# Performance work log

Measured on AMD Instinct MI355X. Metric: run time of the kernel, lower is better.

Reference implementation:

```python
import jax, jax.numpy as jnp
import numpy as np

NUM_TASKS = 5
POOL = 5
R = 8
TOPK = 3
SCALE = 1.0  # module self.scale and forward scale arg, both 1
B, S, DIN, DOUT = 4, 4096, 1024, 1024


def setup_inputs() -> dict:
    key = jax.random.key(0)
    ks = jax.random.split(key, 5)
    inp = {
        "input": jax.random.normal(ks[0], (B, S, DIN), dtype=jnp.float32),
        "W": jax.random.normal(ks[1], (DOUT, DIN), dtype=jnp.float32) / np.sqrt(DIN),
        "lora_down": jax.random.normal(ks[2], (POOL, DIN, R), dtype=jnp.float32) / np.sqrt(DIN),
        "lora_up": jax.random.normal(ks[3], (POOL, R, DOUT), dtype=jnp.float32) / np.sqrt(R),
        "lora_route": jax.random.normal(ks[4], (NUM_TASKS, DIN, POOL), dtype=jnp.float32) * 0.02,
        "task_id": 4,
    }
    return inp


def reference(input, W, lora_down, lora_up, lora_route, task_id):
    # Eval branch (self.training == False), 1 <= task_id <= num_tasks.
    task_id = min(task_id, NUM_TASKS)
    k = min(task_id, TOPK)
    route = lora_route[1]                          # [DIN, POOL] (detach split is a no-op for fwd)
    input_mean = jnp.mean(input, axis=1)           # [B, DIN]
    lora_omegas = jnp.mean(input_mean @ route, axis=0)  # [POOL]
    sliced = lora_omegas[1:task_id + 1]            # source slices from 1
    G, I = jax.lax.top_k(sliced, k)                # indices used DIRECTLY (as in source)
    gate = jax.nn.softmax(G)                       # [k]
    # detached expert products (eval path detaches lora_down @ lora_up)
    dw = jax.lax.stop_gradient(
        jnp.einsum('kdr,kro->kdo', lora_down[I], lora_up[I]))  # [k, DIN, DOUT]
    # delta = sum_i gate[i] * SCALE * (input @ dw[i]); forward scale arg = 1
    delta = SCALE * jnp.einsum('k,bsd,kdo->bso', gate, input, dw)
    # delta_w_all[:B//2] = 0
    bmask = (jnp.arange(input.shape[0]) >= input.shape[0] // 2).astype(delta.dtype)
    delta = delta * bmask[:, None, None]
    return input @ W.T + delta
```

## Files before the change

### kernel.cpp

```cpp
#include <hip/hip_runtime.h>
#include <hip/hip_bf16.h>

typedef __attribute__((ext_vector_type(8))) __bf16 bf16x8;
typedef __attribute__((ext_vector_type(4))) __bf16 bf16x4;
typedef __attribute__((ext_vector_type(4))) float f32x4;

#define DIN 1024
#define DOUT 1024
#define BB 4
#define SS 4096
#define MROWS (BB*SS)
#define POOLN 5
#define RR 8
#define NTASKS 5
#define TOPKK 3

__global__ __launch_bounds__(256) void kA_colsum(const float* __restrict__ in,
                                                 float* __restrict__ partial) {
    const int t = threadIdx.x;
    const int b = blockIdx.x;
    const int idx0 = b * 256 + t;
    const f32x4* __restrict__ inv = (const f32x4*)in;

    float s0 = 0.f, s1 = 0.f, s2 = 0.f, s3 = 0.f;
    size_t idx = idx0;
    f32x4 cur = inv[idx];
#pragma unroll
    for (int i = 0; i < 8; ++i) {
        f32x4 nxt = cur;
        if (i < 7) nxt = inv[idx + 524288];
        s0 += cur[0]; s1 += cur[1]; s2 += cur[2]; s3 += cur[3];
        cur = nxt;
        idx += 524288;
    }
    const int c0 = (t * 4) & (DIN - 1);
    f32x4 p = { s0, s1, s2, s3 };
    *(f32x4*)&partial[(size_t)b * DIN + c0] = p;
}

__global__ __launch_bounds__(256) void k1b_reduce(const float* __restrict__ partial,
                                                  float* __restrict__ partial2) {
    const int tid = blockIdx.x * 256 + threadIdx.x;
    const int c = tid & (DIN - 1);
    const int g = tid >> 10;
    float s = 0.f;
    const int r0 = g * 256;
#pragma unroll 8
    for (int r = r0; r < r0 + 256; ++r)
        s += partial[(size_t)r * DIN + c];
    partial2[(size_t)g * DIN + c] = s;
}

__global__ void k2_gate(const float* __restrict__ partial2,
                        const float* __restrict__ lroute,
                        const int* __restrict__ task_id_p,
                        float* __restrict__ gate, int* __restrict__ gidx) {
    __shared__ float red[4][POOLN];
    const int tix = threadIdx.x;
    const int w = tix >> 6, l = tix & 63;
    float part[POOLN] = {0.f, 0.f, 0.f, 0.f, 0.f};
    for (int d = w * 256 + l; d < w * 256 + 256; d += 64) {
        float cs = 0.f;
#pragma unroll
        for (int g = 0; g < 8; ++g) cs += partial2[g * DIN + d];
        cs *= (1.0f / (float)MROWS);
        const float* rp = &lroute[(size_t)1 * DIN * POOLN + (size_t)d * POOLN];
#pragma unroll
        for (int p = 0; p < POOLN; ++p) part[p] += cs * rp[p];
    }
#pragma unroll
    for (int p = 0; p < POOLN; ++p) {
        float v = part[p];
        for (int off = 32; off; off >>= 1) v += __shfl_down(v, off);
        if (l == 0) red[w][p] = v;
    }
    __syncthreads();
    if (tix == 0) {
#pragma unroll
        for (int p = 0; p < POOLN; ++p)
            part[p] = red[0][p] + red[1][p] + red[2][p] + red[3][p];
        int tid = *task_id_p;
        if (tid > NTASKS) tid = NTASKS;
        int L = tid < (POOLN - 1) ? tid : (POOLN - 1);
        int k = tid < TOPKK ? tid : TOPKK;
        float sl[POOLN];
        for (int j = 0; j < L; ++j) sl[j] = part[1 + j];
        float G[TOPKK]; int I[TOPKK];
        int used = 0;
        for (int j = 0; j < k; ++j) {
            int best = -1; float bv = 0.f;
            for (int i2 = 0; i2 < L; ++i2) {
                if (used & (1 << i2)) continue;
                if (best < 0 || sl[i2] > bv) { bv = sl[i2]; best = i2; }
            }
            used |= 1 << best; G[j] = bv; I[j] = best;
        }
        if (k > 0) {
            float m = G[0];
            float e[TOPKK]; float se = 0.f;
            for (int j = 0; j < k; ++j) { e[j] = expf(G[j] - m); se += e[j]; }
            for (int j = 0; j < k; ++j) { gate[j] = e[j] / se; gidx[j] = I[j]; }
        }
        for (int j = k; j < TOPKK; ++j) { gate[j] = 0.f; gidx[j] = 0; }
    }
}

__global__ __launch_bounds__(256) void k3_weights(const float* __restrict__ W,
                                                  const float* __restrict__ ldown,
                                                  const float* __restrict__ lup,
                                                  const float* __restrict__ gate,
                                                  const int* __restrict__ gidx,
                                                  __bf16* __restrict__ Wb0,
                                                  __bf16* __restrict__ Wb1) {
    const int o = blockIdx.x;
    const int t = threadIdx.x;
    float c[TOPKK][RR];
#pragma unroll
    for (int j = 0; j < TOPKK; ++j) {
        const float g = gate[j];
        const int   p = gidx[j];
#pragma unroll
        for (int r = 0; r < RR; ++r)
            c[j][r] = g * lup[(size_t)p * RR * DOUT + (size_t)r * DOUT + o];
    }
    const int d0 = t * 4;
    const float4 wv = *(const float4*)&W[(size_t)o * DIN + d0];
    float outv[4] = { wv.x, wv.y, wv.z, wv.w };
    float dwv[4]  = { 0.f, 0.f, 0.f, 0.f };
#pragma unroll
    for (int j = 0; j < TOPKK; ++j) {
        const int p = gidx[j];
#pragma unroll
        for (int dd = 0; dd < 4; ++dd) {
            const float4 da = *(const float4*)&ldown[(size_t)p * DIN * RR + (size_t)(d0 + dd) * RR];
            const float4 db = *(const float4*)&ldown[(size_t)p * DIN * RR + (size_t)(d0 + dd) * RR + 4];
            dwv[dd] += da.x * c[j][0] + da.y * c[j][1] + da.z * c[j][2] + da.w * c[j][3]
                     + db.x * c[j][4] + db.y * c[j][5] + db.z * c[j][6] + db.w * c[j][7];
        }
    }
    bf16x4 b0 = { (__bf16)outv[0], (__bf16)outv[1], (__bf16)outv[2], (__bf16)outv[3] };
    bf16x4 b1 = { (__bf16)(outv[0] + dwv[0]), (__bf16)(outv[1] + dwv[1]),
                  (__bf16)(outv[2] + dwv[2]), (__bf16)(outv[3] + dwv[3]) };
    *(bf16x4*)&Wb0[(size_t)o * DIN + d0] = b0;
    *(bf16x4*)&Wb1[(size_t)o * DIN + d0] = b1;
}

__global__ __launch_bounds__(512, 4) void k4_gemm(const float* __restrict__ A,
                                                  const __bf16* __restrict__ B0,
                                                  const __bf16* __restrict__ B1,
                                                  float* __restrict__ C) {
    __shared__ ushort lds[36864];
    const int bid = blockIdx.x;
    const int xcd = bid & 7;
    const int idx = bid >> 3;
    const int tm  = xcd * 16 + (idx >> 2);
    const int tn  = idx & 3;
    const __bf16* __restrict__ Bt = (tm >= 64) ? B1 : B0;

    const int tix  = threadIdx.x;
    const int lane = tix & 63;
    const int wid  = tix >> 6;
    const int wm = wid >> 2, wn = wid & 3;

    const int ar = tix >> 2;
    const int ac = tix & 3;
    const f32x4* __restrict__ pA = (const f32x4*)(A + ((size_t)(tm * 128 + ar)) * 1024 + ac * 8);
    const int awrp  = tix >> 3;
    const int awslot= ((tix & 3) + 4 * ((tix >> 2) & 1)) ^ (awrp & 7);
    const int awoff = awrp * 64 + awslot * 8;

    const int rpl  = lane >> 3;
    const int sl   = (lane & 7) ^ rpl;
    const int srow = rpl * 2 + (sl >> 2);
    const int sc   = sl & 3;
    const char* gB = (const char*)Bt + ((size_t)(tn*256 + wid*32 + srow)) * 2048 + sc * 16;
    const int ldsBst = 4096 + wid * 1024;

    const int rhalf = (lane & 15) >> 1;
    const int slot  = ((lane >> 4) + 4 * (lane & 1)) ^ rhalf;
    const int aoff  = (wm * 32 + rhalf) * 64 + slot * 8;
    const int boff  = 4096 + (wn * 32 + rhalf) * 64 + slot * 8;

    f32x4 acc[4][4];
#pragma unroll
    for (int i = 0; i < 4; ++i)
#pragma unroll
        for (int j = 0; j < 4; ++j) acc[i][j] = (f32x4){0.f, 0.f, 0.f, 0.f};

    auto issueB = [&](int s) {
        const int p = s % 3;
        const size_t kb = (size_t)s * 64;
#pragma unroll
        for (int j = 0; j < 2; ++j) {
            __builtin_amdgcn_global_load_lds(
                (const __attribute__((address_space(1))) void*)(gB + (size_t)j * 32768 + kb),
                (__attribute__((address_space(3))) void*)&lds[p * 12288 + ldsBst + j * 512],
                16, 0, 0);
        }
    };

    auto writeA = [&](int s, f32x4 a0, f32x4 a1) {
        const int p = s % 3;
        bf16x8 v = { (__bf16)a0[0], (__bf16)a0[1], (__bf16)a0[2], (__bf16)a0[3],
                     (__bf16)a1[0], (__bf16)a1[1], (__bf16)a1[2], (__bf16)a1[3] };
        *(bf16x8*)&lds[p * 12288 + awoff] = v;
    };

    auto computeSlab = [&](int s) {
        const int p = s % 3;
        const ushort* aB = &lds[p * 12288 + aoff];
        const ushort* bB = &lds[p * 12288 + boff];
        bf16x8 a[4], b[4];
#pragma unroll
        for (int mi = 0; mi < 4; ++mi) a[mi] = *(const bf16x8*)(aB + mi * 512);
#pragma unroll
        for (int ni = 0; ni < 4; ++ni) b[ni] = *(const bf16x8*)(bB + ni * 512);
        __builtin_amdgcn_s_setprio(1);
#pragma unroll
        for (int mi = 0; mi < 4; ++mi)
#pragma unroll
            for (int ni = 0; ni < 4; ++ni)
                acc[mi][ni] = __builtin_amdgcn_mfma_f32_16x16x32_bf16(
                    a[mi], b[ni], acc[mi][ni], 0, 0, 0);
        __builtin_amdgcn_s_setprio(0);
    };

    f32x4 pa0 = pA[0], pa1 = pA[1];
    issueB(0);
    f32x4 na0 = pA[8], na1 = pA[9];
    issueB(1);
    asm volatile("s_waitcnt vmcnt(6)" ::: "memory");
    writeA(0, pa0, pa1);

#pragma unroll 1
    for (int s = 0; s < 32; ++s) {
        if (s < 31) {
            asm volatile("s_waitcnt vmcnt(2)" ::: "memory");
            writeA(s + 1, na0, na1);
        } else {
            asm volatile("s_waitcnt vmcnt(0)" ::: "memory");
        }
        if (s < 30) {
            na0 = pA[(size_t)(s + 2) * 8];
            na1 = pA[(size_t)(s + 2) * 8 + 1];
            issueB(s + 2);
        }
        asm volatile("s_waitcnt lgkmcnt(0)" ::: "memory");
        __builtin_amdgcn_s_barrier();
        asm volatile("" ::: "memory");
        computeSlab(s);
        asm volatile("" ::: "memory");
        __builtin_amdgcn_s_barrier();
    }

#pragma unroll
    for (int mi = 0; mi < 4; ++mi) {
#pragma unroll
        for (int r = 0; r < 4; ++r) {
            const int grow = tm * 128 + wm * 64 + mi * 16 + (lane >> 4) * 4 + r;
            float* cp = C + (size_t)grow * 1024 + tn * 256 + wn * 64 + (lane & 15);
#pragma unroll
            for (int ni = 0; ni < 4; ++ni) cp[ni * 16] = acc[mi][ni][r];
        }
    }
}

extern "C" void kernel_launch(void* const* d_in, const int* in_sizes, int n_in,
                              void* d_out, int out_size, void* d_ws, size_t ws_size,
                              hipStream_t stream) {
    const float* in     = (const float*)d_in[0];
    const float* W      = (const float*)d_in[1];
    const float* ldown  = (const float*)d_in[2];
    const float* lup    = (const float*)d_in[3];
    const float* lroute = (const float*)d_in[4];
    const int*   taskid = (const int*)d_in[5];
    float* out = (float*)d_out;

    __bf16* Wb0     = (__bf16*)d_ws;
    __bf16* Wb1     = Wb0 + (size_t)DOUT * DIN;
    float*  partial2= (float*)(Wb1 + (size_t)DOUT * DIN);
    float*  gate    = partial2 + 8 * DIN;
    int*    gidx    = (int*)(gate + TOPKK);
    float*  partial = (float*)(gidx + 64);

    kA_colsum<<<2048, 256, 0, stream>>>(in, partial);
    k1b_reduce<<<32, 256, 0, stream>>>(partial, partial2);
    k2_gate<<<1, 256, 0, stream>>>(partial2, lroute, taskid, gate, gidx);
    k3_weights<<<1024, 256, 0, stream>>>(W, ldown, lup, gate, gidx, Wb0, Wb1);
    k4_gemm<<<512, 512, 0, stream>>>(in, Wb0, Wb1, out);
}
```

Baseline: 94.41 us.

## Fuse gate computation into weight-prep kernel and retime LDS waits in GEMM

Folds the single-block gate/top-k kernel into the weight-prep kernel: every block recomputes the route projection and softmax gate in shared memory, which removes one launch and the serial one-block step. The column-sum kernel now keeps two independent load streams in flight per thread. In the GEMM, the LDS wait moves from just before the barrier to the end of the compute slab, so the LDS writes can overlap the global-load issue. The cost is redundant gate work in each of 1024 blocks and a slightly different synchronization order.

```diff
diff --git a/kernel.cpp b/kernel.cpp
--- a/kernel.cpp
+++ b/kernel.cpp
@@ -19,19 +19,25 @@
                                                  float* __restrict__ partial) {
     const int t = threadIdx.x;
     const int b = blockIdx.x;
-    const int idx0 = b * 256 + t;
+    const int tid = b * 256 + t;
     const f32x4* __restrict__ inv = (const f32x4*)in;
 
     float s0 = 0.f, s1 = 0.f, s2 = 0.f, s3 = 0.f;
-    size_t idx = idx0;
-    f32x4 cur = inv[idx];
-#pragma unroll
-    for (int i = 0; i < 8; ++i) {
-        f32x4 nxt = cur;
-        if (i < 7) nxt = inv[idx + 524288];
-        s0 += cur[0]; s1 += cur[1]; s2 += cur[2]; s3 += cur[3];
-        cur = nxt;
-        idx += 524288;
+    size_t ia = (size_t)tid;
+    size_t ib = (size_t)tid + 2097152;
+    f32x4 ca = inv[ia];
+    f32x4 cb = inv[ib];
+#pragma unroll
+    for (int i = 0; i < 4; ++i) {
+        f32x4 na = ca, nb = cb;
+        if (i < 3) {
+            na = inv[ia + 524288];
+            nb = inv[ib + 524288];
+        }
+        s0 += ca[0] + cb[0]; s1 += ca[1] + cb[1];
+        s2 += ca[2] + cb[2]; s3 += ca[3] + cb[3];
+        ca = na; cb = nb;
+        ia += 524288; ib += 524288;
     }
     const int c0 = (t * 4) & (DIN - 1);
     f32x4 p = { s0, s1, s2, s3 };
@@ -51,22 +57,34 @@
     partial2[(size_t)g * DIN + c] = s;
 }
 
-__global__ void k2_gate(const float* __restrict__ partial2,
-                        const float* __restrict__ lroute,
-                        const int* __restrict__ task_id_p,
-                        float* __restrict__ gate, int* __restrict__ gidx) {
+__global__ __launch_bounds__(256) void k23_weights(const float* __restrict__ partial2,
+                                                   const float* __restrict__ lroute,
+                                                   const int* __restrict__ task_id_p,
+                                                   const float* __restrict__ W,
+                                                   const float* __restrict__ ldown,
+                                                   const float* __restrict__ lup,
+                                                   __bf16* __restrict__ Wb0,
+                                                   __bf16* __restrict__ Wb1) {
     __shared__ float red[4][POOLN];
+    __shared__ float sgate[TOPKK];
+    __shared__ int   sgidx[TOPKK];
     const int tix = threadIdx.x;
     const int w = tix >> 6, l = tix & 63;
+
     float part[POOLN] = {0.f, 0.f, 0.f, 0.f, 0.f};
-    for (int d = w * 256 + l; d < w * 256 + 256; d += 64) {
-        float cs = 0.f;
-#pragma unroll
-        for (int g = 0; g < 8; ++g) cs += partial2[g * DIN + d];
-        cs *= (1.0f / (float)MROWS);
-        const float* rp = &lroute[(size_t)1 * DIN * POOLN + (size_t)d * POOLN];
-#pragma unroll
-        for (int p = 0; p < POOLN; ++p) part[p] += cs * rp[p];
+    {
+        const int d0 = tix * 4;
+#pragma unroll
+        for (int dd = 0; dd < 4; ++dd) {
+            const int d = d0 + dd;
+            float cs = 0.f;
+#pragma unroll
+            for (int g = 0; g < 8; ++g) cs += partial2[g * DIN + d];
+            cs *= (1.0f / (float)MROWS);
+            const float* rp = &lroute[(size_t)1 * DIN * POOLN + (size_t)d * POOLN];
+#pragma unroll
+            for (int p = 0; p < POOLN; ++p) part[p] += cs * rp[p];
+        }
     }
 #pragma unroll
     for (int p = 0; p < POOLN; ++p) {
@@ -95,30 +113,26 @@
             }
             used |= 1 << best; G[j] = bv; I[j] = best;
         }
+        float gt[TOPKK] = {0.f, 0.f, 0.f};
+        int   gi[TOPKK] = {0, 0, 0};
         if (k > 0) {
             float m = G[0];
             float e[TOPKK]; float se = 0.f;
             for (int j = 0; j < k; ++j) { e[j] = expf(G[j] - m); se += e[j]; }
-            for (int j = 0; j < k; ++j) { gate[j] = e[j] / se; gidx[j] = I[j]; }
-        }
-        for (int j = k; j < TOPKK; ++j) { gate[j] = 0.f; gidx[j] = 0; }
-    }
-}
-
-__global__ __launch_bounds__(256) void k3_weights(const float* __restrict__ W,
-                                                  const float* __restrict__ ldown,
-                                                  const float* __restrict__ lup,
-                                                  const float* __restrict__ gate,
-                                                  const int* __restrict__ gidx,
-                                                  __bf16* __restrict__ Wb0,
-                                                  __bf16* __restrict__ Wb1) {
+            for (int j = 0; j < k; ++j) { gt[j] = e[j] / se; gi[j] = I[j]; }
+        }
+#pragma unroll
+        for (int j = 0; j < TOPKK; ++j) { sgate[j] = gt[j]; sgidx[j] = gi[j]; }
+    }
+    __syncthreads();
+
     const int o = blockIdx.x;
-    const int t = threadIdx.x;
+    const int t = tix;
     float c[TOPKK][RR];
 #pragma unroll
     for (int j = 0; j < TOPKK; ++j) {
-        const float g = gate[j];
-        const int   p = gidx[j];
+        const float g = sgate[j];
+        const int   p = sgidx[j];
 #pragma unroll
         for (int r = 0; r < RR; ++r)
             c[j][r] = g * lup[(size_t)p * RR * DOUT + (size_t)r * DOUT + o];
@@ -129,7 +143,7 @@
     float dwv[4]  = { 0.f, 0.f, 0.f, 0.f };
 #pragma unroll
     for (int j = 0; j < TOPKK; ++j) {
-        const int p = gidx[j];
+        const int p = sgidx[j];
 #pragma unroll
         for (int dd = 0; dd < 4; ++dd) {
             const float4 da = *(const float4*)&ldown[(size_t)p * DIN * RR + (size_t)(d0 + dd) * RR];
@@ -231,6 +245,7 @@
     issueB(1);
     asm volatile("s_waitcnt vmcnt(6)" ::: "memory");
     writeA(0, pa0, pa1);
+    asm volatile("s_waitcnt lgkmcnt(0)" ::: "memory");
 
 #pragma unroll 1
     for (int s = 0; s < 32; ++s) {
@@ -245,11 +260,11 @@
             na1 = pA[(size_t)(s + 2) * 8 + 1];
             issueB(s + 2);
         }
-        asm volatile("s_waitcnt lgkmcnt(0)" ::: "memory");
         __builtin_amdgcn_s_barrier();
         asm volatile("" ::: "memory");
         computeSlab(s);
         asm volatile("" ::: "memory");
+        asm volatile("s_waitcnt lgkmcnt(0)" ::: "memory");
         __builtin_amdgcn_s_barrier();
     }
 
@@ -279,13 +294,10 @@
     __bf16* Wb0     = (__bf16*)d_ws;
     __bf16* Wb1     = Wb0 + (size_t)DOUT * DIN;
     float*  partial2= (float*)(Wb1 + (size_t)DOUT * DIN);
-    float*  gate    = partial2 + 8 * DIN;
-    int*    gidx    = (int*)(gate + TOPKK);
-    float*  partial = (float*)(gidx + 64);
+    float*  partial = partial2 + 8 * DIN + 64;
 
     kA_colsum<<<2048, 256, 0, stream>>>(in, partial);
     k1b_reduce<<<32, 256, 0, stream>>>(partial, partial2);
-    k2_gate<<<1, 256, 0, stream>>>(partial2, lroute, taskid, gate, gidx);
-    k3_weights<<<1024, 256, 0, stream>>>(W, ldown, lup, gate, gidx, Wb0, Wb1);
+    k23_weights<<<1024, 256, 0, stream>>>(partial2, lroute, taskid, W, ldown, lup, Wb0, Wb1);
     k4_gemm<<<512, 512, 0, stream>>>(in, Wb0, Wb1, out);
 }
```

New measurement: 94.83 us. Within noise of the previous version (+0.4%).

## Fuse all stages into one persistent kernel with software grid barriers

Applied to the files above, without the earlier changes.

Merges the column-sum, reduction, gating, weight-prep and GEMM kernels into a single 512-block launch separated by atomic-counter grid barriers, with a memset to reset the counters. The aim is to remove the launch overhead and tail gaps between five kernels. It also moves the lgkmcnt wait in the GEMM loop to after compute. The fused kernel depends on all 512 blocks being co-resident; if they are not, the spin-wait barriers deadlock. The barriers also make every block wait for the slowest one at each stage.

```diff
diff --git a/kernel.cpp b/kernel.cpp
--- a/kernel.cpp
+++ b/kernel.cpp
@@ -7,260 +7,273 @@
 
 #define DIN 1024
 #define DOUT 1024
-#define BB 4
-#define SS 4096
-#define MROWS (BB*SS)
+#define MROWS 16384
 #define POOLN 5
 #define RR 8
 #define NTASKS 5
 #define TOPKK 3
 
-__global__ __launch_bounds__(256) void kA_colsum(const float* __restrict__ in,
-                                                 float* __restrict__ partial) {
+__device__ __forceinline__ void grid_barrier(unsigned* cnt) {
+    __syncthreads();
+    if (threadIdx.x == 0) {
+        __threadfence();
+        atomicAdd(cnt, 1u);
+        while (__hip_atomic_load(cnt, __ATOMIC_RELAXED, __HIP_MEMORY_SCOPE_AGENT) < 512u)
+            __builtin_amdgcn_s_sleep(2);
+        __threadfence();
+    }
+    __syncthreads();
+}
+
+__global__ __launch_bounds__(512, 4) void kFused(
+        const float* __restrict__ in, const float* __restrict__ W,
+        const float* __restrict__ ldown, const float* __restrict__ lup,
+        const float* __restrict__ lroute, const int* __restrict__ task_id_p,
+        __bf16* __restrict__ Wb0, __bf16* __restrict__ Wb1,
+        float* __restrict__ partial, float* __restrict__ partial2,
+        float* __restrict__ gate, int* __restrict__ gidx,
+        unsigned* __restrict__ cnt, float* __restrict__ C) {
+    __shared__ ushort ldsU[36864];
+    const int b = blockIdx.x;
     const int t = threadIdx.x;
-    const int b = blockIdx.x;
-    const int idx0 = b * 256 + t;
-    const f32x4* __restrict__ inv = (const f32x4*)in;
-
-    float s0 = 0.f, s1 = 0.f, s2 = 0.f, s3 = 0.f;
-    size_t idx = idx0;
-    f32x4 cur = inv[idx];
-#pragma unroll
-    for (int i = 0; i < 8; ++i) {
-        f32x4 nxt = cur;
-        if (i < 7) nxt = inv[idx + 524288];
-        s0 += cur[0]; s1 += cur[1]; s2 += cur[2]; s3 += cur[3];
-        cur = nxt;
-        idx += 524288;
-    }
-    const int c0 = (t * 4) & (DIN - 1);
-    f32x4 p = { s0, s1, s2, s3 };
-    *(f32x4*)&partial[(size_t)b * DIN + c0] = p;
-}
-
-__global__ __launch_bounds__(256) void k1b_reduce(const float* __restrict__ partial,
-                                                  float* __restrict__ partial2) {
-    const int tid = blockIdx.x * 256 + threadIdx.x;
-    const int c = tid & (DIN - 1);
-    const int g = tid >> 10;
-    float s = 0.f;
-    const int r0 = g * 256;
+
+    {
+        const f32x4* __restrict__ inv = (const f32x4*)in;
+        const int tid0 = b * 512 + t;
+        float s0 = 0.f, s1 = 0.f, s2 = 0.f, s3 = 0.f;
+        size_t idx = tid0;
+        f32x4 cur = inv[idx];
+#pragma unroll
+        for (int i = 0; i < 16; ++i) {
+            f32x4 nxt = cur;
+            if (i < 15) nxt = inv[idx + 262144];
+            s0 += cur[0]; s1 += cur[1]; s2 += cur[2]; s3 += cur[3];
+            cur = nxt; idx += 262144;
+        }
+        const int pr = b * 2 + (t >> 8);
+        const int c0 = (t * 4) & (DIN - 1);
+        f32x4 p = { s0, s1, s2, s3 };
+        *(f32x4*)&partial[(size_t)pr * DIN + c0] = p;
+    }
+    grid_barrier(&cnt[0]);
+
+    if (b < 16) {
+        const int tid = b * 512 + t;
+        const int c = tid & (DIN - 1);
+        const int g = tid >> 10;
+        float s = 0.f;
+        const int r0 = g * 128;
 #pragma unroll 8
-    for (int r = r0; r < r0 + 256; ++r)
-        s += partial[(size_t)r * DIN + c];
-    partial2[(size_t)g * DIN + c] = s;
-}
-
-__global__ void k2_gate(const float* __restrict__ partial2,
-                        const float* __restrict__ lroute,
-                        const int* __restrict__ task_id_p,
-                        float* __restrict__ gate, int* __restrict__ gidx) {
-    __shared__ float red[4][POOLN];
-    const int tix = threadIdx.x;
-    const int w = tix >> 6, l = tix & 63;
-    float part[POOLN] = {0.f, 0.f, 0.f, 0.f, 0.f};
-    for (int d = w * 256 + l; d < w * 256 + 256; d += 64) {
-        float cs = 0.f;
-#pragma unroll
-        for (int g = 0; g < 8; ++g) cs += partial2[g * DIN + d];
-        cs *= (1.0f / (float)MROWS);
-        const float* rp = &lroute[(size_t)1 * DIN * POOLN + (size_t)d * POOLN];
-#pragma unroll
-        for (int p = 0; p < POOLN; ++p) part[p] += cs * rp[p];
-    }
-#pragma unroll
-    for (int p = 0; p < POOLN; ++p) {
-        float v = part[p];
-        for (int off = 32; off; off >>= 1) v += __shfl_down(v, off);
-        if (l == 0) red[w][p] = v;
-    }
-    __syncthreads();
-    if (tix == 0) {
-#pragma unroll
-        for (int p = 0; p < POOLN; ++p)
-            part[p] = red[0][p] + red[1][p] + red[2][p] + red[3][p];
-        int tid = *task_id_p;
-        if (tid > NTASKS) tid = NTASKS;
-        int L = tid < (POOLN - 1) ? tid : (POOLN - 1);
-        int k = tid < TOPKK ? tid : TOPKK;
-        float sl[POOLN];
-        for (int j = 0; j < L; ++j) sl[j] = part[1 + j];
-        float G[TOPKK]; int I[TOPKK];
-        int used = 0;
-        for (int j = 0; j < k; ++j) {
-            int best = -1; float bv = 0.f;
-            for (int i2 = 0; i2 < L; ++i2) {
-                if (used & (1 << i2)) continue;
-                if (best < 0 || sl[i2] > bv) { bv = sl[i2]; best = i2; }
-            }
-            used |= 1 << best; G[j] = bv; I[j] = best;
-        }
-        if (k > 0) {
-            float m = G[0];
-            float e[TOPKK]; float se = 0.f;
-            for (int j = 0; j < k; ++j) { e[j] = expf(G[j] - m); se += e[j]; }
-            for (int j = 0; j < k; ++j) { gate[j] = e[j] / se; gidx[j] = I[j]; }
-        }
-        for (int j = k; j < TOPKK; ++j) { gate[j] = 0.f; gidx[j] = 0; }
-    }
-}
-
-__global__ __launch_bounds__(256) void k3_weights(const float* __restrict__ W,
-                                                  const float* __restrict__ ldown,
-                                                  const float* __restrict__ lup,
-                                                  const float* __restrict__ gate,
-                                                  const int* __restrict__ gidx,
-                                                  __bf16* __restrict__ Wb0,
-                                                  __bf16* __restrict__ Wb1) {
-    const int o = blockIdx.x;
-    const int t = threadIdx.x;
-    float c[TOPKK][RR];
-#pragma unroll
-    for (int j = 0; j < TOPKK; ++j) {
-        const float g = gate[j];
-        const int   p = gidx[j];
-#pragma unroll
-        for (int r = 0; r < RR; ++r)
-            c[j][r] = g * lup[(size_t)p * RR * DOUT + (size_t)r * DOUT + o];
-    }
-    const int d0 = t * 4;
-    const float4 wv = *(const float4*)&W[(size_t)o * DIN + d0];
-    float outv[4] = { wv.x, wv.y, wv.z, wv.w };
-    float dwv[4]  = { 0.f, 0.f, 0.f, 0.f };
-#pragma unroll
-    for (int j = 0; j < TOPKK; ++j) {
-        const int p = gidx[j];
-#pragma unroll
-        for (int dd = 0; dd < 4; ++dd) {
-            const float4 da = *(const float4*)&ldown[(size_t)p * DIN * RR + (size_t)(d0 + dd) * RR];
-            const float4 db = *(const float4*)&ldown[(size_t)p * DIN * RR + (size_t)(d0 + dd) * RR + 4];
-            dwv[dd] += da.x * c[j][0] + da.y * c[j][1] + da.z * c[j][2] + da.w * c[j][3]
-                     + db.x * c[j][4] + db.y * c[j][5] + db.z * c[j][6] + db.w * c[j][7];
-        }
-    }
-    bf16x4 b0 = { (__bf16)outv[0], (__bf16)outv[1], (__bf16)outv[2], (__bf16)outv[3] };
-    bf16x4 b1 = { (__bf16)(outv[0] + dwv[0]), (__bf16)(outv[1] + dwv[1]),
-                  (__bf16)(outv[2] + dwv[2]), (__bf16)(outv[3] + dwv[3]) };
-    *(bf16x4*)&Wb0[(size_t)o * DIN + d0] = b0;
-    *(bf16x4*)&Wb1[(size_t)o * DIN + d0] = b1;
-}
-
-__global__ __launch_bounds__(512, 4) void k4_gemm(const float* __restrict__ A,
-                                                  const __bf16* __restrict__ B0,
-                                                  const __bf16* __restrict__ B1,
-                                                  float* __restrict__ C) {
-    __shared__ ushort lds[36864];
-    const int bid = blockIdx.x;
-    const int xcd = bid & 7;
-    const int idx = bid >> 3;
-    const int tm  = xcd * 16 + (idx >> 2);
-    const int tn  = idx & 3;
-    const __bf16* __restrict__ Bt = (tm >= 64) ? B1 : B0;
-
-    const int tix  = threadIdx.x;
-    const int lane = tix & 63;
-    const int wid  = tix >> 6;
-    const int wm = wid >> 2, wn = wid & 3;
-
-    const int ar = tix >> 2;
-    const int ac = tix & 3;
-    const f32x4* __restrict__ pA = (const f32x4*)(A + ((size_t)(tm * 128 + ar)) * 1024 + ac * 8);
-    const int awrp  = tix >> 3;
-    const int awslot= ((tix & 3) + 4 * ((tix >> 2) & 1)) ^ (awrp & 7);
-    const int awoff = awrp * 64 + awslot * 8;
-
-    const int rpl  = lane >> 3;
-    const int sl   = (lane & 7) ^ rpl;
-    const int srow = rpl * 2 + (sl >> 2);
-    const int sc   = sl & 3;
-    const char* gB = (const char*)Bt + ((size_t)(tn*256 + wid*32 + srow)) * 2048 + sc * 16;
-    const int ldsBst = 4096 + wid * 1024;
-
-    const int rhalf = (lane & 15) >> 1;
-    const int slot  = ((lane >> 4) + 4 * (lane & 1)) ^ rhalf;
-    const int aoff  = (wm * 32 + rhalf) * 64 + slot * 8;
-    const int boff  = 4096 + (wn * 32 + rhalf) * 64 + slot * 8;
-
-    f32x4 acc[4][4];
-#pragma unroll
-    for (int i = 0; i < 4; ++i)
-#pragma unroll
-        for (int j = 0; j < 4; ++j) acc[i][j] = (f32x4){0.f, 0.f, 0.f, 0.f};
-
-    auto issueB = [&](int s) {
-        const int p = s % 3;
-        const size_t kb = (size_t)s * 64;
-#pragma unroll
-        for (int j = 0; j < 2; ++j) {
-            __builtin_amdgcn_global_load_lds(
-                (const __attribute__((address_space(1))) void*)(gB + (size_t)j * 32768 + kb),
-                (__attribute__((address_space(3))) void*)&lds[p * 12288 + ldsBst + j * 512],
-                16, 0, 0);
-        }
-    };
-
-    auto writeA = [&](int s, f32x4 a0, f32x4 a1) {
-        const int p = s % 3;
-        bf16x8 v = { (__bf16)a0[0], (__bf16)a0[1], (__bf16)a0[2], (__bf16)a0[3],
-                     (__bf16)a1[0], (__bf16)a1[1], (__bf16)a1[2], (__bf16)a1[3] };
-        *(bf16x8*)&lds[p * 12288 + awoff] = v;
-    };
-
-    auto computeSlab = [&](int s) {
-        const int p = s % 3;
-        const ushort* aB = &lds[p * 12288 + aoff];
-        const ushort* bB = &lds[p * 12288 + boff];
-        bf16x8 a[4], b[4];
-#pragma unroll
-        for (int mi = 0; mi < 4; ++mi) a[mi] = *(const bf16x8*)(aB + mi * 512);
-#pragma unroll
-        for (int ni = 0; ni < 4; ++ni) b[ni] = *(const bf16x8*)(bB + ni * 512);
-        __builtin_amdgcn_s_setprio(1);
-#pragma unroll
-        for (int mi = 0; mi < 4; ++mi)
-#pragma unroll
-            for (int ni = 0; ni < 4; ++ni)
-                acc[mi][ni] = __builtin_amdgcn_mfma_f32_16x16x32_bf16(
-                    a[mi], b[ni], acc[mi][ni], 0, 0, 0);
-        __builtin_amdgcn_s_setprio(0);
-    };
-
-    f32x4 pa0 = pA[0], pa1 = pA[1];
-    issueB(0);
-    f32x4 na0 = pA[8], na1 = pA[9];
-    issueB(1);
-    asm volatile("s_waitcnt vmcnt(6)" ::: "memory");
-    writeA(0, pa0, pa1);
+        for (int r = r0; r < r0 + 128; ++r) s += partial[(size_t)r * DIN + c];
+        partial2[(size_t)g * DIN + c] = s;
+    }
+    grid_barrier(&cnt[1]);
+
+    if (b == 0) {
+        float (*red)[POOLN] = (float(*)[POOLN])ldsU;
+        if (t < 256) {
+            const int w = t >> 6, l = t & 63;
+            float part[POOLN] = {0.f, 0.f, 0.f, 0.f, 0.f};
+            for (int d = w * 256 + l; d < w * 256 + 256; d += 64) {
+                float cs = 0.f;
+#pragma unroll
+                for (int g = 0; g < 8; ++g) cs += partial2[g * DIN + d];
+                cs *= (1.0f / (float)MROWS);
+                const float* rp = &lroute[(size_t)1 * DIN * POOLN + (size_t)d * POOLN];
+#pragma unroll
+                for (int p = 0; p < POOLN; ++p) part[p] += cs * rp[p];
+            }
+#pragma unroll
+            for (int p = 0; p < POOLN; ++p) {
+                float v = part[p];
+                for (int off = 32; off; off >>= 1) v += __shfl_down(v, off);
+                if (l == 0) red[w][p] = v;
+            }
+        }
+        __syncthreads();
+        if (t == 0) {
+            float part[POOLN];
+#pragma unroll
+            for (int p = 0; p < POOLN; ++p)
+                part[p] = red[0][p] + red[1][p] + red[2][p] + red[3][p];
+            int tid = *task_id_p;
+            if (tid > NTASKS) tid = NTASKS;
+            int L = tid < (POOLN - 1) ? tid : (POOLN - 1);
+            int k = tid < TOPKK ? tid : TOPKK;
+            float sl[POOLN];
+            for (int j = 0; j < L; ++j) sl[j] = part[1 + j];
+            float G[TOPKK]; int I[TOPKK];
+            int used = 0;
+            for (int j = 0; j < k; ++j) {
+                int best = -1; float bv = 0.f;
+                for (int i2 = 0; i2 < L; ++i2) {
+                    if (used & (1 << i2)) continue;
+                    if (best < 0 || sl[i2] > bv) { bv = sl[i2]; best = i2; }
+                }
+                used |= 1 << best; G[j] = bv; I[j] = best;
+            }
+            float gt[TOPKK] = {0.f, 0.f, 0.f};
+            int   gi[TOPKK] = {0, 0, 0};
+            if (k > 0) {
+                float m = G[0];
+                float e[TOPKK]; float se = 0.f;
+                for (int j = 0; j < k; ++j) { e[j] = expf(G[j] - m); se += e[j]; }
+                for (int j = 0; j < k; ++j) { gt[j] = e[j] / se; gi[j] = I[j]; }
+            }
+#pragma unroll
+            for (int j = 0; j < TOPKK; ++j) { gate[j] = gt[j]; gidx[j] = gi[j]; }
+        }
+    }
+    grid_barrier(&cnt[2]);
+
+    {
+        const int o = 2 * b + (t >> 8);
+        const int tl = t & 255;
+        float c[TOPKK][RR];
+#pragma unroll
+        for (int j = 0; j < TOPKK; ++j) {
+            const float g = gate[j];
+            const int   p = gidx[j];
+#pragma unroll
+            for (int r = 0; r < RR; ++r)
+                c[j][r] = g * lup[(size_t)p * RR * DOUT + (size_t)r * DOUT + o];
+        }
+        const int d0 = tl * 4;
+        const float4 wv = *(const float4*)&W[(size_t)o * DIN + d0];
+        float outv[4] = { wv.x, wv.y, wv.z, wv.w };
+        float dwv[4]  = { 0.f, 0.f, 0.f, 0.f };
+#pragma unroll
+        for (int j = 0; j < TOPKK; ++j) {
+            const int p = gidx[j];
+#pragma unroll
+            for (int dd = 0; dd < 4; ++dd) {
+                const float4 da = *(const float4*)&ldown[(size_t)p * DIN * RR + (size_t)(d0 + dd) * RR];
+                const float4 db = *(const float4*)&ldown[(size_t)p * DIN * RR + (size_t)(d0 + dd) * RR + 4];
+                dwv[dd] += da.x * c[j][0] + da.y * c[j][1] + da.z * c[j][2] + da.w * c[j][3]
+                         + db.x * c[j][4] + db.y * c[j][5] + db.z * c[j][6] + db.w * c[j][7];
+            }
+        }
+        bf16x4 b0 = { (__bf16)outv[0], (__bf16)outv[1], (__bf16)outv[2], (__bf16)outv[3] };
+        bf16x4 b1 = { (__bf16)(outv[0] + dwv[0]), (__bf16)(outv[1] + dwv[1]),
+                      (__bf16)(outv[2] + dwv[2]), (__bf16)(outv[3] + dwv[3]) };
+        *(bf16x4*)&Wb0[(size_t)o * DIN + d0] = b0;
+        *(bf16x4*)&Wb1[(size_t)o * DIN + d0] = b1;
+    }
+    grid_barrier(&cnt[3]);
+
+    {
+        ushort* lds = ldsU;
+        const int bid = b;
+        const int xcd = bid & 7;
+        const int idx = bid >> 3;
+        const int tm  = xcd * 16 + (idx >> 2);
+        const int tn  = idx & 3;
+        const __bf16* __restrict__ Bt = (tm >= 64) ? Wb1 : Wb0;
+
+        const int tix  = t;
+        const int lane = tix & 63;
+        const int wid  = tix >> 6;
+        const int wm = wid >> 2, wn = wid & 3;
+
+        const int ar = tix >> 2;
+        const int ac = tix & 3;
+        const f32x4* __restrict__ pA = (const f32x4*)(in + ((size_t)(tm * 128 + ar)) * 1024 + ac * 8);
+        const int awrp  = tix >> 3;
+        const int awslot= ((tix & 3) + 4 * ((tix >> 2) & 1)) ^ (awrp & 7);
+        const int awoff = awrp * 64 + awslot * 8;
+
+        const int rpl  = lane >> 3;
+        const int sl   = (lane & 7) ^ rpl;
+        const int srow = rpl * 2 + (sl >> 2);
+        const int sc   = sl & 3;
+        const char* gB = (const char*)Bt + ((size_t)(tn*256 + wid*32 + srow)) * 2048 + sc * 16;
+        const int ldsBst = 4096 + wid * 1024;
+
+        const int rhalf = (lane & 15) >> 1;
+        const int slot  = ((lane >> 4) + 4 * (lane & 1)) ^ rhalf;
+        const int aoff  = (wm * 32 + rhalf) * 64 + slot * 8;
+        const int boff  = 4096 + (wn * 32 + rhalf) * 64 + slot * 8;
+
+        f32x4 acc[4][4];
+#pragma unroll
+        for (int i = 0; i < 4; ++i)
+#pragma unroll
+            for (int j = 0; j < 4; ++j) acc[i][j] = (f32x4){0.f, 0.f, 0.f, 0.f};
+
+        auto issueB = [&](int s) {
+            const int p = s % 3;
+            const size_t kb = (size_t)s * 64;
+#pragma unroll
+            for (int j = 0; j < 2; ++j) {
+                __builtin_amdgcn_global_load_lds(
+                    (const __attribute__((address_space(1))) void*)(gB + (size_t)j * 32768 + kb),
+                    (__attribute__((address_space(3))) void*)&lds[p * 12288 + ldsBst + j * 512],
+                    16, 0, 0);
+            }
+        };
+        auto writeA = [&](int s, f32x4 a0, f32x4 a1) {
+            const int p = s % 3;
+            bf16x8 v = { (__bf16)a0[0], (__bf16)a0[1], (__bf16)a0[2], (__bf16)a0[3],
+                         (__bf16)a1[0], (__bf16)a1[1], (__bf16)a1[2], (__bf16)a1[3] };
+            *(bf16x8*)&lds[p * 12288 + awoff] = v;
+        };
+        auto computeSlab = [&](int s) {
+            const int p = s % 3;
+            const ushort* aB = &lds[p * 12288 + aoff];
+            const ushort* bB = &lds[p * 12288 + boff];
+            bf16x8 a[4], bb[4];
+#pragma unroll
+            for (int mi = 0; mi < 4; ++mi) a[mi] = *(const bf16x8*)(aB + mi * 512);
+#pragma unroll
+            for (int ni = 0; ni < 4; ++ni) bb[ni] = *(const bf16x8*)(bB + ni * 512);
+            __builtin_amdgcn_s_setprio(1);
+#pragma unroll
+            for (int mi = 0; mi < 4; ++mi)
+#pragma unroll
+                for (int ni = 0; ni < 4; ++ni)
+                    acc[mi][ni] = __builtin_amdgcn_mfma_f32_16x16x32_bf16(
+                        a[mi], bb[ni], acc[mi][ni], 0, 0, 0);
+            __builtin_amdgcn_s_setprio(0);
+        };
+
+        f32x4 pa0 = pA[0], pa1 = pA[1];
+        issueB(0);
+        f32x4 na0 = pA[8], na1 = pA[9];
+        issueB(1);
+        asm volatile("s_waitcnt vmcnt(6)" ::: "memory");
+        writeA(0, pa0, pa1);
+        asm volatile("s_waitcnt lgkmcnt(0)" ::: "memory");
 
 #pragma unroll 1
-    for (int s = 0; s < 32; ++s) {
-        if (s < 31) {
-            asm volatile("s_waitcnt vmcnt(2)" ::: "memory");
-            writeA(s + 1, na0, na1);
-        } else {
-            asm volatile("s_waitcnt vmcnt(0)" ::: "memory");
-        }
-        if (s < 30) {
-            na0 = pA[(size_t)(s + 2) * 8];
-            na1 = pA[(size_t)(s + 2) * 8 + 1];
-            issueB(s + 2);
-        }
-        asm volatile("s_waitcnt lgkmcnt(0)" ::: "memory");
-        __builtin_amdgcn_s_barrier();
-        asm volatile("" ::: "memory");
-        computeSlab(s);
-        asm volatile("" ::: "memory");
-        __builtin_amdgcn_s_barrier();
-    }
-
-#pragma unroll
-    for (int mi = 0; mi < 4; ++mi) {
-#pragma unroll
-        for (int r = 0; r < 4; ++r) {
-            const int grow = tm * 128 + wm * 64 + mi * 16 + (lane >> 4) * 4 + r;
-            float* cp = C + (size_t)grow * 1024 + tn * 256 + wn * 64 + (lane & 15);
-#pragma unroll
-            for (int ni = 0; ni < 4; ++ni) cp[ni * 16] = acc[mi][ni][r];
+        for (int s = 0; s < 32; ++s) {
+            if (s < 31) {
+                asm volatile("s_waitcnt vmcnt(2)" ::: "memory");
+                writeA(s + 1, na0, na1);
+            } else {
+                asm volatile("s_waitcnt vmcnt(0)" ::: "memory");
+            }
+            if (s < 30) {
+                na0 = pA[(size_t)(s + 2) * 8];
+                na1 = pA[(size_t)(s + 2) * 8 + 1];
+                issueB(s + 2);
+            }
+            __builtin_amdgcn_s_barrier();
+            asm volatile("" ::: "memory");
+            computeSlab(s);
+            asm volatile("" ::: "memory");
+            asm volatile("s_waitcnt lgkmcnt(0)" ::: "memory");
+            __builtin_amdgcn_s_barrier();
+        }
+
+#pragma unroll
+        for (int mi = 0; mi < 4; ++mi) {
+#pragma unroll
+            for (int r = 0; r < 4; ++r) {
+                const int grow = tm * 128 + wm * 64 + mi * 16 + (lane >> 4) * 4 + r;
+                float* cp = C + (size_t)grow * 1024 + tn * 256 + wn * 64 + (lane & 15);
+#pragma unroll
+                for (int ni = 0; ni < 4; ++ni) cp[ni * 16] = acc[mi][ni][r];
+            }
         }
     }
 }
@@ -276,16 +289,16 @@
     const int*   taskid = (const int*)d_in[5];
     float* out = (float*)d_out;
 
-    __bf16* Wb0     = (__bf16*)d_ws;
-    __bf16* Wb1     = Wb0 + (size_t)DOUT * DIN;
-    float*  partial2= (float*)(Wb1 + (size_t)DOUT * DIN);
-    float*  gate    = partial2 + 8 * DIN;
-    int*    gidx    = (int*)(gate + TOPKK);
-    float*  partial = (float*)(gidx + 64);
-
-    kA_colsum<<<2048, 256, 0, stream>>>(in, partial);
-    k1b_reduce<<<32, 256, 0, stream>>>(partial, partial2);
-    k2_gate<<<1, 256, 0, stream>>>(partial2, lroute, taskid, gate, gidx);
-    k3_weights<<<1024, 256, 0, stream>>>(W, ldown, lup, gate, gidx, Wb0, Wb1);
-    k4_gemm<<<512, 512, 0, stream>>>(in, Wb0, Wb1, out);
+    __bf16*   Wb0      = (__bf16*)d_ws;
+    __bf16*   Wb1      = Wb0 + (size_t)DOUT * DIN;
+    float*    partial2 = (float*)(Wb1 + (size_t)DOUT * DIN);
+    float*    gate     = partial2 + 8 * DIN;
+    int*      gidx     = (int*)(gate + 16);
+    unsigned* cnt      = (unsigned*)(gidx + 16);
+    float*    partial  = (float*)(cnt + 16);
+
+    hipMemsetAsync(cnt, 0, 16 * sizeof(unsigned), stream);
+    kFused<<<512, 512, 0, stream>>>(in, W, ldown, lup, lroute, taskid,
+                                    Wb0, Wb1, partial, partial2, gate, gidx,
+                                    cnt, out);
 }
```

Measured after the change: 265.2 us. +180.9%, slower.
